# Optimization experiments

Measured on AMD Instinct MI355X. Metric: run time of the kernel, lower is better.

## Reference

```python
import jax, jax.numpy as jnp
import numpy as np

B, N_PATTS, D_PATTS, L_PATTS, L_SEQ = 32, 32, 12, 32, 1024
L_OUT = 32
RHO = 1.0
BIG = 1e30  # stands in for +inf at DP boundaries (finite to keep grads clean)


def setup_inputs() -> dict:
    key = jax.random.key(0)
    kx, kp = jax.random.split(key)
    x = jax.random.normal(kx, (B, D_PATTS, L_SEQ), dtype=jnp.float32)
    patts = jax.random.normal(kp, (N_PATTS, D_PATTS, L_PATTS), dtype=jnp.float32)
    return {"x": x, "patts": patts}


def _pairwise_sqdist(x, patts):
    # cost[b,n,i,j] = sum_d (patts[n,d,i] - x[b,d,j])^2, shape [B,N,P,L]
    x2 = jnp.sum(x * x, axis=1)            # [B,L]
    p2 = jnp.sum(patts * patts, axis=1)    # [N,P]
    cross = jnp.einsum('bdl,ndp->bnpl', x, patts)  # [B,N,P,L]
    return p2[None, :, :, None] + x2[:, None, None, :] - 2.0 * cross


def _dp_column(a, c, w):
    # Solve cur[i] = c[i] + min(a[i], w*cur[i-1]) sequentially over pattern axis.
    # a, c: [B,N,P]; returns [B,N,P]
    a_t = jnp.moveaxis(a, -1, 0)  # [P,B,N]
    c_t = jnp.moveaxis(c, -1, 0)

    def step(cur_prev, ac):
        a_i, c_i = ac
        cur = c_i + jnp.minimum(a_i, w * cur_prev)
        return cur, cur

    init = jnp.full(c.shape[:-1], BIG, c.dtype)  # no row above the first
    _, cur = jax.lax.scan(step, init, (a_t, c_t))
    return jnp.moveaxis(cur, 0, -1)


def _dtw_dp(cost, w):
    # Weighted DTW recurrence:
    #   D[i,j] = cost[i,j] + min(D[i-1,j-1], w*D[i-1,j], w*D[i,j-1])
    # with D[0,0] = cost[0,0] and out-of-range predecessors = +inf.
    # cost: [B,N,P,L] -> D: [B,N,P,L]
    Bb, Nn, P, L = cost.shape
    cost_t = jnp.moveaxis(cost, -1, 0)  # [L,B,N,P]

    # first column j=0: D[i,0] = c[i,0] + w*D[i-1,0], D[0,0] = c[0,0]
    a0 = jnp.where(jnp.arange(P) == 0, 0.0, BIG).astype(cost.dtype)
    a0 = jnp.broadcast_to(a0, cost.shape[:3])
    d0 = _dp_column(a0, cost_t[0], w)  # [B,N,P]

    def outer_step(d_prev, c_col):
        # prev_shift[i] = D[i-1, j-1]; boundary row is +inf for j >= 1
        top = jnp.full_like(d_prev[..., :1], BIG)
        prev_shift = jnp.concatenate([top, d_prev[..., :-1]], axis=-1)
        a = jnp.minimum(prev_shift, w * d_prev)
        cur = _dp_column(a, c_col, w)
        return cur, cur

    _, rest = jax.lax.scan(outer_step, d0, cost_t[1:])  # [L-1,B,N,P]
    D = jnp.concatenate([d0[None], rest], axis=0)       # [L,B,N,P]
    return jnp.moveaxis(D, 0, -1)                       # [B,N,P,L]


def reference(x, patts):
    w = RHO ** (1.0 / L_PATTS)
    cost = _pairwise_sqdist(x, patts)   # [B,N,P,L]
    D = _dtw_dp(cost, w)                # [B,N,P,L]
    return D[..., -L_OUT:]              # [B,N,P,L_OUT]
```

## Files before the change

kernel.cpp:

```cpp
#include <hip/hip_runtime.h>


#define BIGF 1e30f
#define LL   1024
#define LOUT 32

using v4f = __attribute__((ext_vector_type(4))) float;

template<int CTRL>
__device__ __forceinline__ float dpp_self(float v) {
    return __int_as_float(__builtin_amdgcn_update_dpp(
        __float_as_int(v), __float_as_int(v), CTRL, 0xF, 0xF, false));
}
template<int CTRL>
__device__ __forceinline__ float dpp_zero(float v) {
    return __int_as_float(__builtin_amdgcn_update_dpp(
        0, __float_as_int(v), CTRL, 0xF, 0xF, false));
}
template<int CTRL, int RM>
__device__ __forceinline__ float dpp_self_rm(float v) {
    return __int_as_float(__builtin_amdgcn_update_dpp(
        __float_as_int(v), __float_as_int(v), CTRL, RM, 0xF, false));
}
template<int CTRL, int RM>
__device__ __forceinline__ float dpp_zero_rm(float v) {
    return __int_as_float(__builtin_amdgcn_update_dpp(
        0, __float_as_int(v), CTRL, RM, 0xF, false));
}
__device__ __forceinline__ float wshr1z(float v) {
    return __int_as_float(__builtin_amdgcn_update_dpp(
        0, __float_as_int(v), 0x138 , 0xF, 0xF, false));
}
__device__ __forceinline__ float rdlane(float v, int l) {
    return __int_as_float(__builtin_amdgcn_readlane(__float_as_int(v), l));
}

__device__ __forceinline__ float scan_min64(float t) {
    t = fminf(t, dpp_self<0x111>(t));
    t = fminf(t, dpp_self<0x112>(t));
    t = fminf(t, dpp_self<0x114>(t));
    t = fminf(t, dpp_self<0x118>(t));
    t = fminf(t, dpp_self_rm<0x142, 0xA>(t));
    t = fminf(t, dpp_self_rm<0x143, 0xC>(t));
    return t;
}
__device__ __forceinline__ float scan_add64(float t) {
    t += dpp_zero<0x111>(t);
    t += dpp_zero<0x112>(t);
    t += dpp_zero<0x114>(t);
    t += dpp_zero<0x118>(t);
    t += dpp_zero_rm<0x142, 0xA>(t);
    t += dpp_zero_rm<0x143, 0xC>(t);
    return t;
}

__global__ __launch_bounds__(64)
__attribute__((amdgpu_waves_per_eu(1, 1)))
void dtw_kernel(const float* __restrict__ x, const float* __restrict__ patts,
                float* __restrict__ out) {
    const int lane = threadIdx.x;
    const bool l0  = (lane == 0);
    const int blk  = blockIdx.x;
    const int b    = blk >> 5, n = blk & 31;
    const float* __restrict__ xb = x + b * (12 * LL);
    const float* __restrict__ pn = patts + n * (12 * 32);

    float prm[12], p2r;
    {
        const int r = lane & 31;
        float s2 = 0.f;
#pragma unroll
        for (int d = 0; d < 12; ++d) {
            float v = pn[d * 32 + r];
            s2 = fmaf(v, v, s2);
            prm[d] = -2.0f * v;
        }
        p2r = s2;
    }

    float SX[12][16];
#pragma unroll
    for (int d = 0; d < 12; ++d) {
#pragma unroll
        for (int c = 0; c < 4; ++c) {
            v4f v = *(const v4f*)(xb + d * LL + 16 * lane + 4 * c);
            SX[d][4 * c + 0] = v.x;
            SX[d][4 * c + 1] = v.y;
            SX[d][4 * c + 2] = v.z;
            SX[d][4 * c + 3] = v.w;
        }
    }
    float SX2[16];
#pragma unroll
    for (int k = 0; k < 16; ++k) {
        float t = SX[0][k] * SX[0][k];
#pragma unroll
        for (int d = 1; d < 12; ++d) t = fmaf(SX[d][k], SX[d][k], t);
        SX2[k] = t;
    }
#pragma unroll
    for (int d = 0; d < 12; ++d) {
        float run = 0.f;
#pragma unroll
        for (int k = 0; k < 16; ++k) { run += SX[d][k]; SX[d][k] = run; }
        float ex = scan_add64(run) - run;
#pragma unroll
        for (int k = 0; k < 16; ++k) SX[d][k] += ex;
    }
    {
        float run = 0.f;
#pragma unroll
        for (int k = 0; k < 16; ++k) { run += SX2[k]; SX2[k] = run; }
        float ex = scan_add64(run) - run;
#pragma unroll
        for (int k = 0; k < 16; ++k) SX2[k] += ex;
    }
    float jp1[16];
#pragma unroll
    for (int k = 0; k < 16; ++k) jp1[k] = (float)(16 * lane + k + 1);

    float S[16], Dp[16];

    {
        float pv[12], p2u;
#pragma unroll
        for (int d = 0; d < 12; ++d) pv[d] = rdlane(prm[d], 0);
        p2u = rdlane(p2r, 0);
#pragma unroll
        for (int k = 0; k < 16; ++k) S[k] = fmaf(p2u, jp1[k], SX2[k]);
#pragma unroll
        for (int d = 0; d < 12; ++d)
#pragma unroll
            for (int k = 0; k < 16; ++k) S[k] = fmaf(pv[d], SX[d][k], S[k]);
#pragma unroll
        for (int k = 0; k < 16; ++k) Dp[k] = S[k];
        if (lane >= 62) {
            float* ob = out + blk * (32 * LOUT) + (lane - 62) * 16;
#pragma unroll
            for (int c = 0; c < 4; ++c) {
                v4f v = {Dp[4*c], Dp[4*c+1], Dp[4*c+2], Dp[4*c+3]};
                *(v4f*)(ob + 4 * c) = v;
            }
        }
    }

#pragma unroll 2
    for (int i = 1; i < 32; ++i) {
        float pv[12], p2u;
#pragma unroll
        for (int d = 0; d < 12; ++d) pv[d] = rdlane(prm[d], i);
        p2u = rdlane(p2r, i);

#pragma unroll
        for (int k = 0; k < 16; ++k) S[k] = fmaf(p2u, jp1[k], SX2[k]);
#pragma unroll
        for (int d = 0; d < 12; ++d)
#pragma unroll
            for (int k = 0; k < 16; ++k) S[k] = fmaf(pv[d], SX[d][k], S[k]);

        float dsh = wshr1z(Dp[15]); dsh = l0 ? BIGF : dsh;
        float se  = wshr1z(S[15]);

        float m[16];
        m[0] = fminf(dsh, Dp[0]) - se;
#pragma unroll
        for (int k = 1; k < 16; ++k)
            m[k] = fminf(m[k-1], fminf(Dp[k-1], Dp[k]) - S[k-1]);

        float t  = scan_min64(m[15]);
        float te = wshr1z(t); te = l0 ? BIGF : te;

#pragma unroll
        for (int k = 0; k < 16; ++k)
            Dp[k] = S[k] + fminf(te, m[k]);

        if (lane >= 62) {
            float* ob = out + blk * (32 * LOUT) + (lane - 62) * 16;
#pragma unroll
            for (int c = 0; c < 4; ++c) {
                v4f v = {Dp[4*c], Dp[4*c+1], Dp[4*c+2], Dp[4*c+3]};
                *(v4f*)(ob + i * 32 + 4 * c) = v;
            }
        }
    }
}

extern "C" void kernel_launch(void* const* d_in, const int* in_sizes, int n_in,
                              void* d_out, int out_size, void* d_ws, size_t ws_size,
                              hipStream_t stream) {
    const float* x     = (const float*)d_in[0];
    const float* patts = (const float*)d_in[1];
    float* out         = (float*)d_out;
    dtw_kernel<<<dim3(1024), dim3(64), 0, stream>>>(x, patts, out);
}
```

Measured before the change: 78.64 us.

## Software-pipeline next row's cost computation into current row's min-scan chain

Splits the per-row cost computation S into chunks and interleaves them with the dependent DPP min-scan of the current row, using ping-pong S buffers. The within-lane prefix min is restructured into four independent groups of four, shortening the serial fminf chain. The aim is to hide the latency of the cross-lane DPP scan and the serial recurrence behind independent FMA work. It costs an extra 16-register buffer, which adds register pressure on a single-wave kernel.

```diff
diff --git a/kernel.cpp b/kernel.cpp
--- a/kernel.cpp
+++ b/kernel.cpp
@@ -119,70 +119,89 @@
 #pragma unroll
     for (int k = 0; k < 16; ++k) jp1[k] = (float)(16 * lane + k + 1);
 
-    float S[16], Dp[16];
-
-    {
-        float pv[12], p2u;
-#pragma unroll
-        for (int d = 0; d < 12; ++d) pv[d] = rdlane(prm[d], 0);
-        p2u = rdlane(p2r, 0);
-#pragma unroll
-        for (int k = 0; k < 16; ++k) S[k] = fmaf(p2u, jp1[k], SX2[k]);
-#pragma unroll
-        for (int d = 0; d < 12; ++d)
-#pragma unroll
-            for (int k = 0; k < 16; ++k) S[k] = fmaf(pv[d], SX[d][k], S[k]);
-#pragma unroll
-        for (int k = 0; k < 16; ++k) Dp[k] = S[k];
-        if (lane >= 62) {
-            float* ob = out + blk * (32 * LOUT) + (lane - 62) * 16;
-#pragma unroll
-            for (int c = 0; c < 4; ++c) {
-                v4f v = {Dp[4*c], Dp[4*c+1], Dp[4*c+2], Dp[4*c+3]};
-                *(v4f*)(ob + 4 * c) = v;
-            }
-        }
-    }
-
-#pragma unroll 2
-    for (int i = 1; i < 32; ++i) {
-        float pv[12], p2u;
-#pragma unroll
-        for (int d = 0; d < 12; ++d) pv[d] = rdlane(prm[d], i);
-        p2u = rdlane(p2r, i);
-
-#pragma unroll
-        for (int k = 0; k < 16; ++k) S[k] = fmaf(p2u, jp1[k], SX2[k]);
-#pragma unroll
-        for (int d = 0; d < 12; ++d)
-#pragma unroll
-            for (int k = 0; k < 16; ++k) S[k] = fmaf(pv[d], SX[d][k], S[k]);
-
-        float dsh = wshr1z(Dp[15]); dsh = l0 ? BIGF : dsh;
-        float se  = wshr1z(S[15]);
-
-        float m[16];
-        m[0] = fminf(dsh, Dp[0]) - se;
-#pragma unroll
-        for (int k = 1; k < 16; ++k)
-            m[k] = fminf(m[k-1], fminf(Dp[k-1], Dp[k]) - S[k-1]);
-
-        float t  = scan_min64(m[15]);
-        float te = wshr1z(t); te = l0 ? BIGF : te;
-
-#pragma unroll
-        for (int k = 0; k < 16; ++k)
-            Dp[k] = S[k] + fminf(te, m[k]);
-
-        if (lane >= 62) {
-            float* ob = out + blk * (32 * LOUT) + (lane - 62) * 16;
-#pragma unroll
-            for (int c = 0; c < 4; ++c) {
-                v4f v = {Dp[4*c], Dp[4*c+1], Dp[4*c+2], Dp[4*c+3]};
-                *(v4f*)(ob + i * 32 + 4 * c) = v;
-            }
-        }
-    }
+    float SA[16], SB[16], Dp[16];
+
+#define SN_CHUNK0(SN, inx) do { \
+    float p2u = rdlane(p2r, (inx)); \
+    _Pragma("unroll") for (int k = 0; k < 16; ++k) \
+        SN[k] = fmaf(p2u, jp1[k], SX2[k]); \
+    _Pragma("unroll") for (int d = 0; d < 3; ++d) { \
+        float pv = rdlane(prm[d], (inx)); \
+        _Pragma("unroll") for (int k = 0; k < 16; ++k) \
+            SN[k] = fmaf(pv, SX[d][k], SN[k]); \
+    } \
+} while (0)
+
+#define SN_CHUNKD(SN, inx, d0, d1) do { \
+    _Pragma("unroll") for (int d = (d0); d < (d1); ++d) { \
+        float pv = rdlane(prm[d], (inx)); \
+        _Pragma("unroll") for (int k = 0; k < 16; ++k) \
+            SN[k] = fmaf(pv, SX[d][k], SN[k]); \
+    } \
+} while (0)
+
+#define COMPUTE_S_FULL(SN, inx) do { \
+    SN_CHUNK0(SN, (inx)); SN_CHUNKD(SN, (inx), 3, 12); \
+} while (0)
+
+#define STORE_ROW(i) do { \
+    if (lane >= 62) { \
+        float* ob = out + blk * (32 * LOUT) + (lane - 62) * 16; \
+        _Pragma("unroll") for (int c = 0; c < 4; ++c) { \
+            v4f v = {Dp[4*c], Dp[4*c+1], Dp[4*c+2], Dp[4*c+3]}; \
+            *(v4f*)(ob + (i) * 32 + 4 * c) = v; \
+        } \
+    } \
+} while (0)
+
+#define ROW_CHAIN(i, SC, SN, CN) do { \
+    float dsh = wshr1z(Dp[15]); dsh = l0 ? BIGF : dsh; \
+    float se  = wshr1z(SC[15]); \
+    float z[16]; \
+    z[0] = fminf(dsh, Dp[0]) - se; \
+    _Pragma("unroll") for (int k = 1; k < 16; ++k) \
+        z[k] = fminf(Dp[k-1], Dp[k]) - SC[k-1]; \
+    if (CN) { SN_CHUNK0(SN, (i) + 1); } \
+    _Pragma("unroll") for (int g = 0; g < 4; ++g) { \
+        _Pragma("unroll") for (int j = 1; j < 4; ++j) \
+            z[4*g + j] = fminf(z[4*g + j - 1], z[4*g + j]); \
+    } \
+    if (CN) { SN_CHUNKD(SN, (i) + 1, 3, 6); } \
+    float e1 = z[3]; \
+    float e2 = fminf(e1, z[7]); \
+    float e3 = fminf(e2, z[11]); \
+    float m15 = fminf(e3, z[15]); \
+    float t = scan_min64(m15); \
+    if (CN) { SN_CHUNKD(SN, (i) + 1, 6, 9); } \
+    float te = wshr1z(t); te = l0 ? BIGF : te; \
+    float te1 = fminf(te, e1), te2 = fminf(te, e2), te3 = fminf(te, e3); \
+    _Pragma("unroll") for (int k = 0;  k < 4;  ++k) Dp[k] = SC[k] + fminf(te,  z[k]); \
+    _Pragma("unroll") for (int k = 4;  k < 8;  ++k) Dp[k] = SC[k] + fminf(te1, z[k]); \
+    _Pragma("unroll") for (int k = 8;  k < 12; ++k) Dp[k] = SC[k] + fminf(te2, z[k]); \
+    _Pragma("unroll") for (int k = 12; k < 16; ++k) Dp[k] = SC[k] + fminf(te3, z[k]); \
+    if (CN) { SN_CHUNKD(SN, (i) + 1, 9, 12); } \
+    STORE_ROW(i); \
+} while (0)
+
+    COMPUTE_S_FULL(SA, 0);
+#pragma unroll
+    for (int k = 0; k < 16; ++k) Dp[k] = SA[k];
+    STORE_ROW(0);
+    COMPUTE_S_FULL(SB, 1);
+
+#pragma unroll 1
+    for (int kk = 0; kk < 15; ++kk) {
+        const int i0 = 2 * kk + 1;
+        ROW_CHAIN(i0,     SB, SA, true);
+        ROW_CHAIN(i0 + 1, SA, SB, true);
+    }
+    ROW_CHAIN(31, SB, SA, false);
+
+#undef SN_CHUNK0
+#undef SN_CHUNKD
+#undef COMPUTE_S_FULL
+#undef STORE_ROW
+#undef ROW_CHAIN
 }
 
 extern "C" void kernel_launch(void* const* d_in, const int* in_sizes, int n_in,
```

Result: no change. 78.59 us (-0.1%).

## Split DTW columns across two waves with LDS flag-based row pipelining

Applied to the files above, without the earlier changes.

Each block now uses two wavefronts, each owning half of the 1024 sequence columns (8 per lane instead of 16). Wave 0 handles the left half and publishes a boundary package per pattern row (its min-scan carry, last S, last D) into LDS behind a flag. Wave 1 spin-waits on that flag and folds the carry into its own scan, so the two waves run as a staggered pipeline. The aim is to halve per-wave register work and the serial FMA chain per row, at the cost of LDS spin-wait synchronization, a dependency delay between waves, and extra prefix-sum fixup through LDS.

```diff
diff --git a/kernel.cpp b/kernel.cpp
--- a/kernel.cpp
+++ b/kernel.cpp
@@ -54,17 +54,23 @@
     return t;
 }
 
-__global__ __launch_bounds__(64)
-__attribute__((amdgpu_waves_per_eu(1, 1)))
+__global__ __launch_bounds__(128, 2)
 void dtw_kernel(const float* __restrict__ x, const float* __restrict__ patts,
                 float* __restrict__ out) {
-    const int lane = threadIdx.x;
+    const int tid  = threadIdx.x;
+    const int lane = tid & 63;
+    const int wv   = tid >> 6;
     const bool l0  = (lane == 0);
     const int blk  = blockIdx.x;
     const int b    = blk >> 5, n = blk & 31;
     const float* __restrict__ xb = x + b * (12 * LL);
     const float* __restrict__ pn = patts + n * (12 * 32);
 
+    __shared__ float ldsT[13];
+    __shared__ float pkgf[32][4];
+
+    if (tid < 32) pkgf[tid][3] = 0.0f;
+
     float prm[12], p2r;
     {
         const int r = lane & 31;
@@ -78,21 +84,18 @@
         p2r = s2;
     }
 
-    float SX[12][16];
+    const int colbase = (wv << 9) + (lane << 3);
+    float SX[12][8];
 #pragma unroll
     for (int d = 0; d < 12; ++d) {
-#pragma unroll
-        for (int c = 0; c < 4; ++c) {
-            v4f v = *(const v4f*)(xb + d * LL + 16 * lane + 4 * c);
-            SX[d][4 * c + 0] = v.x;
-            SX[d][4 * c + 1] = v.y;
-            SX[d][4 * c + 2] = v.z;
-            SX[d][4 * c + 3] = v.w;
-        }
-    }
-    float SX2[16];
-#pragma unroll
-    for (int k = 0; k < 16; ++k) {
+        v4f a = *(const v4f*)(xb + d * LL + colbase);
+        v4f c = *(const v4f*)(xb + d * LL + colbase + 4);
+        SX[d][0] = a.x; SX[d][1] = a.y; SX[d][2] = a.z; SX[d][3] = a.w;
+        SX[d][4] = c.x; SX[d][5] = c.y; SX[d][6] = c.z; SX[d][7] = c.w;
+    }
+    float SX2[8];
+#pragma unroll
+    for (int k = 0; k < 8; ++k) {
         float t = SX[0][k] * SX[0][k];
 #pragma unroll
         for (int d = 1; d < 12; ++d) t = fmaf(SX[d][k], SX[d][k], t);
@@ -102,87 +105,132 @@
     for (int d = 0; d < 12; ++d) {
         float run = 0.f;
 #pragma unroll
-        for (int k = 0; k < 16; ++k) { run += SX[d][k]; SX[d][k] = run; }
-        float ex = scan_add64(run) - run;
-#pragma unroll
-        for (int k = 0; k < 16; ++k) SX[d][k] += ex;
+        for (int k = 0; k < 8; ++k) { run += SX[d][k]; SX[d][k] = run; }
+        float inc = scan_add64(run);
+        if (wv == 0 && lane == 63) ldsT[d] = inc;
+        float ex = inc - run;
+#pragma unroll
+        for (int k = 0; k < 8; ++k) SX[d][k] += ex;
     }
     {
         float run = 0.f;
 #pragma unroll
-        for (int k = 0; k < 16; ++k) { run += SX2[k]; SX2[k] = run; }
-        float ex = scan_add64(run) - run;
-#pragma unroll
-        for (int k = 0; k < 16; ++k) SX2[k] += ex;
-    }
-    float jp1[16];
-#pragma unroll
-    for (int k = 0; k < 16; ++k) jp1[k] = (float)(16 * lane + k + 1);
-
-    float S[16], Dp[16];
-
-    {
-        float pv[12], p2u;
-#pragma unroll
-        for (int d = 0; d < 12; ++d) pv[d] = rdlane(prm[d], 0);
-        p2u = rdlane(p2r, 0);
-#pragma unroll
-        for (int k = 0; k < 16; ++k) S[k] = fmaf(p2u, jp1[k], SX2[k]);
-#pragma unroll
-        for (int d = 0; d < 12; ++d)
-#pragma unroll
-            for (int k = 0; k < 16; ++k) S[k] = fmaf(pv[d], SX[d][k], S[k]);
-#pragma unroll
-        for (int k = 0; k < 16; ++k) Dp[k] = S[k];
-        if (lane >= 62) {
-            float* ob = out + blk * (32 * LOUT) + (lane - 62) * 16;
-#pragma unroll
-            for (int c = 0; c < 4; ++c) {
-                v4f v = {Dp[4*c], Dp[4*c+1], Dp[4*c+2], Dp[4*c+3]};
-                *(v4f*)(ob + 4 * c) = v;
-            }
-        }
-    }
-
-#pragma unroll 2
-    for (int i = 1; i < 32; ++i) {
-        float pv[12], p2u;
-#pragma unroll
-        for (int d = 0; d < 12; ++d) pv[d] = rdlane(prm[d], i);
-        p2u = rdlane(p2r, i);
-
-#pragma unroll
-        for (int k = 0; k < 16; ++k) S[k] = fmaf(p2u, jp1[k], SX2[k]);
-#pragma unroll
-        for (int d = 0; d < 12; ++d)
-#pragma unroll
-            for (int k = 0; k < 16; ++k) S[k] = fmaf(pv[d], SX[d][k], S[k]);
-
-        float dsh = wshr1z(Dp[15]); dsh = l0 ? BIGF : dsh;
-        float se  = wshr1z(S[15]);
-
-        float m[16];
-        m[0] = fminf(dsh, Dp[0]) - se;
-#pragma unroll
-        for (int k = 1; k < 16; ++k)
-            m[k] = fminf(m[k-1], fminf(Dp[k-1], Dp[k]) - S[k-1]);
-
-        float t  = scan_min64(m[15]);
-        float te = wshr1z(t); te = l0 ? BIGF : te;
-
-#pragma unroll
-        for (int k = 0; k < 16; ++k)
-            Dp[k] = S[k] + fminf(te, m[k]);
-
-        if (lane >= 62) {
-            float* ob = out + blk * (32 * LOUT) + (lane - 62) * 16;
-#pragma unroll
-            for (int c = 0; c < 4; ++c) {
-                v4f v = {Dp[4*c], Dp[4*c+1], Dp[4*c+2], Dp[4*c+3]};
-                *(v4f*)(ob + i * 32 + 4 * c) = v;
-            }
-        }
-    }
+        for (int k = 0; k < 8; ++k) { run += SX2[k]; SX2[k] = run; }
+        float inc = scan_add64(run);
+        if (wv == 0 && lane == 63) ldsT[12] = inc;
+        float ex = inc - run;
+#pragma unroll
+        for (int k = 0; k < 8; ++k) SX2[k] += ex;
+    }
+    __syncthreads();
+    if (wv == 1) {
+#pragma unroll
+        for (int d = 0; d < 12; ++d) {
+            float off = ldsT[d];
+#pragma unroll
+            for (int k = 0; k < 8; ++k) SX[d][k] += off;
+        }
+        float off2 = ldsT[12];
+#pragma unroll
+        for (int k = 0; k < 8; ++k) SX2[k] += off2;
+    }
+    float jp1[8];
+#pragma unroll
+    for (int k = 0; k < 8; ++k) jp1[k] = (float)(colbase + k + 1);
+
+    float S[8], Dp[8];
+
+#define COMPUTE_S(i) do { \
+    float p2u = rdlane(p2r, (i)); \
+    _Pragma("unroll") for (int k = 0; k < 8; ++k) \
+        S[k] = fmaf(p2u, jp1[k], SX2[k]); \
+    _Pragma("unroll") for (int d = 0; d < 12; ++d) { \
+        float pv = rdlane(prm[d], (i)); \
+        _Pragma("unroll") for (int k = 0; k < 8; ++k) \
+            S[k] = fmaf(pv, SX[d][k], S[k]); \
+    } \
+} while (0)
+
+#define PUBLISH(i, Zv) do { \
+    if (lane == 63) { \
+        pkgf[i][0] = (Zv); pkgf[i][1] = S[7]; pkgf[i][2] = Dp[7]; \
+        asm volatile("s_waitcnt lgkmcnt(0)" ::: "memory"); \
+        *(volatile int*)&pkgf[i][3] = (i) + 1; \
+    } \
+} while (0)
+
+#define STORE_ROW(i) do { \
+    if (lane >= 60) { \
+        float* ob = out + blk * (32 * LOUT) + (i) * LOUT + (lane - 60) * 8; \
+        v4f va = {Dp[0], Dp[1], Dp[2], Dp[3]}; \
+        v4f vb = {Dp[4], Dp[5], Dp[6], Dp[7]}; \
+        *(v4f*)ob = va; *(v4f*)(ob + 4) = vb; \
+    } \
+} while (0)
+
+    if (wv == 0) {
+        COMPUTE_S(0);
+#pragma unroll
+        for (int k = 0; k < 8; ++k) Dp[k] = S[k];
+        PUBLISH(0, BIGF);
+#pragma unroll 1
+        for (int i = 1; i < 32; ++i) {
+            COMPUTE_S(i);
+            float dsh = wshr1z(Dp[7]); dsh = l0 ? BIGF : dsh;
+            float se  = wshr1z(S[7]);
+            float m[8];
+            m[0] = fminf(dsh, Dp[0]) - se;
+#pragma unroll
+            for (int k = 1; k < 8; ++k)
+                m[k] = fminf(m[k-1], fminf(Dp[k-1], Dp[k]) - S[k-1]);
+            float t  = scan_min64(m[7]);
+            float te = wshr1z(t); te = l0 ? BIGF : te;
+#pragma unroll
+            for (int k = 0; k < 8; ++k) Dp[k] = S[k] + fminf(te, m[k]);
+            PUBLISH(i, t);
+        }
+    } else {
+        COMPUTE_S(0);
+#pragma unroll
+        for (int k = 0; k < 8; ++k) Dp[k] = S[k];
+        STORE_ROW(0);
+        float Db;
+        {
+            volatile int* fl = (volatile int*)&pkgf[0][3];
+            int cnt = 0;
+            while (*fl != 1) { if (++cnt > 1000000) break; __builtin_amdgcn_s_sleep(2); }
+            asm volatile("" ::: "memory");
+            Db = pkgf[0][2];
+        }
+#pragma unroll 1
+        for (int i = 1; i < 32; ++i) {
+            COMPUTE_S(i);
+            volatile int* fl = (volatile int*)&pkgf[i][3];
+            int cnt = 0;
+            while (*fl != i + 1) { if (++cnt > 1000000) break; __builtin_amdgcn_s_sleep(2); }
+            asm volatile("" ::: "memory");
+            float Z  = pkgf[i][0];
+            float Sb = pkgf[i][1];
+            float dsh = wshr1z(Dp[7]); dsh = l0 ? Db : dsh;
+            float se  = wshr1z(S[7]);  se  = l0 ? Sb : se;
+            float m[8];
+            m[0] = fminf(dsh, Dp[0]) - se;
+#pragma unroll
+            for (int k = 1; k < 8; ++k)
+                m[k] = fminf(m[k-1], fminf(Dp[k-1], Dp[k]) - S[k-1]);
+            float t  = scan_min64(m[7]);
+            float te = wshr1z(t); te = l0 ? BIGF : te;
+            te = fminf(te, Z);
+#pragma unroll
+            for (int k = 0; k < 8; ++k) Dp[k] = S[k] + fminf(te, m[k]);
+            Db = pkgf[i][2];
+            STORE_ROW(i);
+        }
+    }
+
+#undef COMPUTE_S
+#undef PUBLISH
+#undef STORE_ROW
 }
 
 extern "C" void kernel_launch(void* const* d_in, const int* in_sizes, int n_in,
@@ -191,5 +239,5 @@
     const float* x     = (const float*)d_in[0];
     const float* patts = (const float*)d_in[1];
     float* out         = (float*)d_out;
-    dtw_kernel<<<dim3(1024), dim3(64), 0, stream>>>(x, patts, out);
-}
+    dtw_kernel<<<dim3(1024), dim3(128), 0, stream>>>(x, patts, out);
+}
```

Measured after the change: 82.65 us. +5.1%, slower.
